# Optimization experiments

Hardware: AMD Instinct MI355X
Metric: run time of the kernel (lower is better)

## Reference

```python
import jax, jax.numpy as jnp
import numpy as np


def setup_inputs() -> dict:
    key = jax.random.key(0)
    k1, k2, k3 = jax.random.split(key, 3)
    N, C, H, W, K = 4, 128, 40, 30, 64
    return {
        "x": jax.random.normal(k1, (N, C, H, W), dtype=jnp.float32),
        "conv_w": jax.random.normal(k2, (K, C), dtype=jnp.float32) * 0.1,  # 1x1 conv weight [K,C,1,1] squeezed
        "centroids": jax.random.uniform(k3, (K, C), dtype=jnp.float32),
        "patch_size": 5,
        "stride": 1,
    }


def reference(x, conv_w, centroids, patch_size, stride):
    N, C, H, W = x.shape
    K = centroids.shape[0]
    # descriptor-wise L2 normalization (torch F.normalize semantics, eps=1e-12)
    norm = jnp.sqrt(jnp.sum(x * x, axis=1, keepdims=True))
    xn = x / jnp.maximum(norm, 1e-12)
    # 1x1 conv (no bias) + softmax over clusters -> soft assignment [N,K,H,W]
    logits = jnp.einsum('nchw,kc->nkhw', xn, conv_w)
    sa = jax.nn.softmax(logits, axis=1)
    # residuals [N,K,C,H,W]: (x - c_k) * a_k, then flatten K,C
    res = (xn[:, None, :, :, :] - centroids[None, :, :, None, None]) * sa[:, :, None, :, :]
    res = res.reshape(N, K * C, H, W)
    # 2D integral image with top-left zero padding -> [N,KC,H+1,W+1]
    I = jnp.cumsum(jnp.cumsum(res, axis=-1), axis=-2)
    I = jnp.pad(I, ((0, 0), (0, 0), (1, 0), (1, 0)))
    # box-filter via integral-image differencing (equivalent to the grouped
    # dilated 2x2 conv with weights [[+1,-1],[-1,+1]], stride=s, dilation=p)
    p, s = int(patch_size), int(stride)
    out = (I[:, :, p::s, p::s] - I[:, :, p::s, :-p:s]
           - I[:, :, :-p:s, p::s] + I[:, :, :-p:s, :-p:s])
    return out / (p * p)
```

## Files before the change

### kernel.cpp

```cpp
#include <hip/hip_runtime.h>

#define C_ 128
#define K_ 64
#define H_ 40
#define W_ 30
#define N_ 4
#define HW_ 1200
#define P_ 5
#define OH_ 36
#define OW_ 26
#define OHW_ 936

template<int CTRL>
__device__ __forceinline__ float dpp0f(float v) {
  return __int_as_float(__builtin_amdgcn_update_dpp(
      0, __float_as_int(v), CTRL, 0xF, 0xF, true));
}
__device__ __forceinline__ float swz_x16(float v) {
  return __int_as_float(__builtin_amdgcn_ds_swizzle(__float_as_int(v), 0x401F));
}

__global__ __launch_bounds__(256) void k1_prep(
    const float* __restrict__ x, const float* __restrict__ cw,
    float* __restrict__ xn, float* __restrict__ sa)
{
  __shared__ float xs[C_][32];
  __shared__ float wt[C_][K_];
  __shared__ float part[8][32];
  __shared__ float ls[K_][32];
  __shared__ float rnorm_s[32];
  __shared__ float rsum_s[32];

  const int tid  = threadIdx.x;
  const int pix0 = blockIdx.x << 5;

  for (int e = tid; e < C_*K_; e += 256) {
    const int c = e >> 6, kk = e & 63;
    wt[c][kk] = cw[kk*C_ + c];
  }
  for (int e = tid; e < C_*32; e += 256) {
    const int c = e >> 5, pl = e & 31;
    const int pix = pix0 + pl;
    const int n = pix / HW_, rem = pix - n*HW_;
    xs[c][pl] = x[(size_t)(n*C_ + c)*HW_ + rem];
  }
  __syncthreads();
  {
    const int pl = tid & 31, cq = tid >> 5;
    float s = 0.f;
    #pragma unroll
    for (int cc = 0; cc < 16; ++cc) {
      const float v = xs[cq*16 + cc][pl];
      s = fmaf(v, v, s);
    }
    part[cq][pl] = s;
  }
  __syncthreads();
  if (tid < 32) {
    float s = 0.f;
    #pragma unroll
    for (int qq = 0; qq < 8; ++qq) s += part[qq][tid];
    rnorm_s[tid] = 1.f / fmaxf(sqrtf(s), 1e-12f);
  }
  __syncthreads();
  {
    const int pl = tid & 31, kq = tid >> 5;
    float acc[8];
    #pragma unroll
    for (int qq = 0; qq < 8; ++qq) acc[qq] = 0.f;
    for (int c = 0; c < C_; ++c) {
      const float xv = xs[c][pl];
      const float4 w0 = *(const float4*)&wt[c][kq*8];
      const float4 w1 = *(const float4*)&wt[c][kq*8 + 4];
      acc[0] = fmaf(xv, w0.x, acc[0]);
      acc[1] = fmaf(xv, w0.y, acc[1]);
      acc[2] = fmaf(xv, w0.z, acc[2]);
      acc[3] = fmaf(xv, w0.w, acc[3]);
      acc[4] = fmaf(xv, w1.x, acc[4]);
      acc[5] = fmaf(xv, w1.y, acc[5]);
      acc[6] = fmaf(xv, w1.z, acc[6]);
      acc[7] = fmaf(xv, w1.w, acc[7]);
    }
    const float rn = rnorm_s[pl];
    #pragma unroll
    for (int qq = 0; qq < 8; ++qq) ls[kq*8 + qq][pl] = acc[qq] * rn;
  }
  __syncthreads();
  if (tid < 32) {
    const int pl = tid;
    float m = -1e30f;
    for (int kk = 0; kk < K_; ++kk) m = fmaxf(m, ls[kk][pl]);
    float s = 0.f;
    for (int kk = 0; kk < K_; ++kk) {
      const float e = expf(ls[kk][pl] - m);
      ls[kk][pl] = e;
      s += e;
    }
    rsum_s[pl] = 1.f / s;
  }
  __syncthreads();
  for (int e = tid; e < K_*32; e += 256) {
    const int kk = e >> 5, pl = e & 31;
    const int pix = pix0 + pl;
    const int n = pix / HW_, rem = pix - n*HW_;
    sa[(size_t)(n*K_ + kk)*HW_ + rem] = ls[kk][pl] * rsum_s[pl];
  }
  for (int e = tid; e < C_*32; e += 256) {
    const int c = e >> 5, pl = e & 31;
    const int pix = pix0 + pl;
    const int n = pix / HW_, rem = pix - n*HW_;
    xn[(size_t)(n*C_ + c)*HW_ + rem] = xs[c][pl] * rnorm_s[pl];
  }
}

__global__ __launch_bounds__(256) void k2_box(
    const float* __restrict__ xn, const float* __restrict__ sa,
    const float* __restrict__ cent, float* __restrict__ out)
{
  const int tid = threadIdx.x;
  const int w   = tid & 31;
  const int wc  = (w < W_) ? w : (W_ - 1);
  const int c   = (blockIdx.x << 3) + (tid >> 5);
  const int k   = blockIdx.y;
  const int n   = blockIdx.z;

  const float cv = cent[k*C_ + c];
  const float* __restrict__ xp = xn + (size_t)(n*C_ + c)*HW_ + wc;
  const float* __restrict__ sp = sa + (size_t)(n*K_ + k)*HW_ + wc;

  float q[H_];
  #pragma unroll
  for (int h = 0; h < H_; ++h) {
    q[h] = (xp[h*W_] - cv) * sp[h*W_];
  }

  float vq = q[0] + q[1] + q[2] + q[3] + q[4];
  float* __restrict__ op = out + (size_t)((n*K_ + k)*C_ + c)*OHW_ + w;

  #pragma unroll
  for (int i = 0; i < OH_; ++i) {
    const float sw = swz_x16(vq);
    float hs = vq;
    hs += dpp0f<0x101>(vq) + dpp0f<0x11F>(sw);
    hs += dpp0f<0x102>(vq) + dpp0f<0x11E>(sw);
    hs += dpp0f<0x103>(vq) + dpp0f<0x11D>(sw);
    hs += dpp0f<0x104>(vq) + dpp0f<0x11C>(sw);
    if (w < OW_) op[i*OW_] = hs * (1.f / (P_*P_));
    if (i < OH_ - 1) vq += q[i + P_] - q[i];
  }
}

extern "C" void kernel_launch(void* const* d_in, const int* in_sizes, int n_in,
                              void* d_out, int out_size, void* d_ws, size_t ws_size,
                              hipStream_t stream) {
  const float* x  = (const float*)d_in[0];
  const float* cw = (const float*)d_in[1];
  const float* ce = (const float*)d_in[2];

  float* xn = (float*)d_ws;
  float* sa = xn + (size_t)N_*C_*HW_;
  float* out = (float*)d_out;

  k1_prep<<<dim3(150), dim3(256), 0, stream>>>(x, cw, xn, sa);
  k2_box<<<dim3(C_/8, K_, N_), dim3(256), 0, stream>>>(xn, sa, ce, out);
}
```

Measured before the change: 46.37 us.

## Restructure prep kernel to 4-pixel blocks with shuffle reductions; fold 1/25 scale

The prep kernel now assigns 4 pixels per block across 1200 blocks instead of 32 pixels across 150. The L2 norm, the logit dot products and the softmax use wave shuffle reductions, and x is read straight from global memory as float4 instead of being staged in LDS. The 1/25 box scale is folded into xn and the centroid, which removes the final multiply in the box kernel. Output stores become nontemporal and the DPP adds are reordered. More blocks improve occupancy on the small prep stage, but x is read from global memory twice and the weights are reloaded by every block.

```diff
diff --git a/kernel.cpp b/kernel.cpp
--- a/kernel.cpp
+++ b/kernel.cpp
@@ -10,6 +10,7 @@
 #define OH_ 36
 #define OW_ 26
 #define OHW_ 936
+#define INV25 (1.0f/25.0f)
 
 template<int CTRL>
 __device__ __forceinline__ float dpp0f(float v) {
@@ -24,92 +25,98 @@
     const float* __restrict__ x, const float* __restrict__ cw,
     float* __restrict__ xn, float* __restrict__ sa)
 {
-  __shared__ float xs[C_][32];
-  __shared__ float wt[C_][K_];
-  __shared__ float part[8][32];
-  __shared__ float ls[K_][32];
-  __shared__ float rnorm_s[32];
-  __shared__ float rsum_s[32];
+  __shared__ float wt[K_][132];
+  __shared__ float ls[K_][5];
 
   const int tid  = threadIdx.x;
-  const int pix0 = blockIdx.x << 5;
+  const int bid  = blockIdx.x;
+  const int n    = bid / 300;
+  const int rem  = (bid - n*300) * 4;
+  const float* __restrict__ xb = x + (size_t)n*C_*HW_ + rem;
 
-  for (int e = tid; e < C_*K_; e += 256) {
-    const int c = e >> 6, kk = e & 63;
-    wt[c][kk] = cw[kk*C_ + c];
+  for (int e = tid; e < K_*C_/4; e += 256) {
+    const int k  = e >> 5;
+    const int c4 = (e & 31) << 2;
+    const float4 v = *(const float4*)(cw + k*C_ + c4);
+    *(float4*)&wt[k][c4] = v;
   }
-  for (int e = tid; e < C_*32; e += 256) {
-    const int c = e >> 5, pl = e & 31;
-    const int pix = pix0 + pl;
-    const int n = pix / HW_, rem = pix - n*HW_;
-    xs[c][pl] = x[(size_t)(n*C_ + c)*HW_ + rem];
+
+  const int lane = tid & 63;
+  const int wv   = tid >> 6;
+  const float4 a0 = *(const float4*)(xb + (size_t)lane*HW_);
+  const float4 a1 = *(const float4*)(xb + (size_t)(lane + 64)*HW_);
+  float sx = a0.x*a0.x + a1.x*a1.x;
+  float sy = a0.y*a0.y + a1.y*a1.y;
+  float sz = a0.z*a0.z + a1.z*a1.z;
+  float sw = a0.w*a0.w + a1.w*a1.w;
+  #pragma unroll
+  for (int m = 1; m < 64; m <<= 1) {
+    sx += __shfl_xor(sx, m, 64);
+    sy += __shfl_xor(sy, m, 64);
+    sz += __shfl_xor(sz, m, 64);
+    sw += __shfl_xor(sw, m, 64);
+  }
+  const float rnx = 1.f / fmaxf(sqrtf(sx), 1e-12f);
+  const float rny = 1.f / fmaxf(sqrtf(sy), 1e-12f);
+  const float rnz = 1.f / fmaxf(sqrtf(sz), 1e-12f);
+  const float rnw = 1.f / fmaxf(sqrtf(sw), 1e-12f);
+
+  if (wv == 0) {
+    float4 o;
+    o.x = a0.x*rnx*INV25; o.y = a0.y*rny*INV25;
+    o.z = a0.z*rnz*INV25; o.w = a0.w*rnw*INV25;
+    *(float4*)(xn + ((size_t)n*C_ + lane)*HW_ + rem) = o;
+  } else if (wv == 1) {
+    float4 o;
+    o.x = a1.x*rnx*INV25; o.y = a1.y*rny*INV25;
+    o.z = a1.z*rnz*INV25; o.w = a1.w*rnw*INV25;
+    *(float4*)(xn + ((size_t)n*C_ + lane + 64)*HW_ + rem) = o;
+  }
+
+  __syncthreads();
+
+  const int k  = tid >> 2;
+  const int cq = tid & 3;
+  const float* __restrict__ xc = xb + (size_t)cq*32*HW_;
+  float ax = 0.f, ay = 0.f, az = 0.f, aw = 0.f;
+  #pragma unroll
+  for (int j = 0; j < 8; ++j) {
+    const float4 w4 = *(const float4*)&wt[k][cq*32 + j*4];
+    const float4 x0 = *(const float4*)(xc + (size_t)(j*4 + 0)*HW_);
+    const float4 x1 = *(const float4*)(xc + (size_t)(j*4 + 1)*HW_);
+    const float4 x2 = *(const float4*)(xc + (size_t)(j*4 + 2)*HW_);
+    const float4 x3 = *(const float4*)(xc + (size_t)(j*4 + 3)*HW_);
+    ax = fmaf(w4.x, x0.x, ax); ay = fmaf(w4.x, x0.y, ay);
+    az = fmaf(w4.x, x0.z, az); aw = fmaf(w4.x, x0.w, aw);
+    ax = fmaf(w4.y, x1.x, ax); ay = fmaf(w4.y, x1.y, ay);
+    az = fmaf(w4.y, x1.z, az); aw = fmaf(w4.y, x1.w, aw);
+    ax = fmaf(w4.z, x2.x, ax); ay = fmaf(w4.z, x2.y, ay);
+    az = fmaf(w4.z, x2.z, az); aw = fmaf(w4.z, x2.w, aw);
+    ax = fmaf(w4.w, x3.x, ax); ay = fmaf(w4.w, x3.y, ay);
+    az = fmaf(w4.w, x3.z, az); aw = fmaf(w4.w, x3.w, aw);
+  }
+  ax += __shfl_xor(ax, 1, 64); ax += __shfl_xor(ax, 2, 64);
+  ay += __shfl_xor(ay, 1, 64); ay += __shfl_xor(ay, 2, 64);
+  az += __shfl_xor(az, 1, 64); az += __shfl_xor(az, 2, 64);
+  aw += __shfl_xor(aw, 1, 64); aw += __shfl_xor(aw, 2, 64);
+  if (cq == 0) {
+    ls[k][0] = ax * rnx;
+    ls[k][1] = ay * rny;
+    ls[k][2] = az * rnz;
+    ls[k][3] = aw * rnw;
   }
   __syncthreads();
+
   {
-    const int pl = tid & 31, cq = tid >> 5;
-    float s = 0.f;
+    const float v = ls[lane][wv];
+    float mx = v;
     #pragma unroll
-    for (int cc = 0; cc < 16; ++cc) {
-      const float v = xs[cq*16 + cc][pl];
-      s = fmaf(v, v, s);
-    }
-    part[cq][pl] = s;
-  }
-  __syncthreads();
-  if (tid < 32) {
-    float s = 0.f;
+    for (int m = 1; m < 64; m <<= 1) mx = fmaxf(mx, __shfl_xor(mx, m, 64));
+    const float e = expf(v - mx);
+    float s = e;
     #pragma unroll
-    for (int qq = 0; qq < 8; ++qq) s += part[qq][tid];
-    rnorm_s[tid] = 1.f / fmaxf(sqrtf(s), 1e-12f);
-  }
-  __syncthreads();
-  {
-    const int pl = tid & 31, kq = tid >> 5;
-    float acc[8];
-    #pragma unroll
-    for (int qq = 0; qq < 8; ++qq) acc[qq] = 0.f;
-    for (int c = 0; c < C_; ++c) {
-      const float xv = xs[c][pl];
-      const float4 w0 = *(const float4*)&wt[c][kq*8];
-      const float4 w1 = *(const float4*)&wt[c][kq*8 + 4];
-      acc[0] = fmaf(xv, w0.x, acc[0]);
-      acc[1] = fmaf(xv, w0.y, acc[1]);
-      acc[2] = fmaf(xv, w0.z, acc[2]);
-      acc[3] = fmaf(xv, w0.w, acc[3]);
-      acc[4] = fmaf(xv, w1.x, acc[4]);
-      acc[5] = fmaf(xv, w1.y, acc[5]);
-      acc[6] = fmaf(xv, w1.z, acc[6]);
-      acc[7] = fmaf(xv, w1.w, acc[7]);
-    }
-    const float rn = rnorm_s[pl];
-    #pragma unroll
-    for (int qq = 0; qq < 8; ++qq) ls[kq*8 + qq][pl] = acc[qq] * rn;
-  }
-  __syncthreads();
-  if (tid < 32) {
-    const int pl = tid;
-    float m = -1e30f;
-    for (int kk = 0; kk < K_; ++kk) m = fmaxf(m, ls[kk][pl]);
-    float s = 0.f;
-    for (int kk = 0; kk < K_; ++kk) {
-      const float e = expf(ls[kk][pl] - m);
-      ls[kk][pl] = e;
-      s += e;
-    }
-    rsum_s[pl] = 1.f / s;
-  }
-  __syncthreads();
-  for (int e = tid; e < K_*32; e += 256) {
-    const int kk = e >> 5, pl = e & 31;
-    const int pix = pix0 + pl;
-    const int n = pix / HW_, rem = pix - n*HW_;
-    sa[(size_t)(n*K_ + kk)*HW_ + rem] = ls[kk][pl] * rsum_s[pl];
-  }
-  for (int e = tid; e < C_*32; e += 256) {
-    const int c = e >> 5, pl = e & 31;
-    const int pix = pix0 + pl;
-    const int n = pix / HW_, rem = pix - n*HW_;
-    xn[(size_t)(n*C_ + c)*HW_ + rem] = xs[c][pl] * rnorm_s[pl];
+    for (int m = 1; m < 64; m <<= 1) s += __shfl_xor(s, m, 64);
+    sa[((size_t)n*K_ + lane)*HW_ + rem + wv] = e / s;
   }
 }
 
@@ -124,14 +131,14 @@
   const int k   = blockIdx.y;
   const int n   = blockIdx.z;
 
-  const float cv = cent[k*C_ + c];
+  const float cv25 = cent[k*C_ + c] * INV25;
   const float* __restrict__ xp = xn + (size_t)(n*C_ + c)*HW_ + wc;
   const float* __restrict__ sp = sa + (size_t)(n*K_ + k)*HW_ + wc;
 
   float q[H_];
   #pragma unroll
   for (int h = 0; h < H_; ++h) {
-    q[h] = (xp[h*W_] - cv) * sp[h*W_];
+    q[h] = (xp[h*W_] - cv25) * sp[h*W_];
   }
 
   float vq = q[0] + q[1] + q[2] + q[3] + q[4];
@@ -141,11 +148,15 @@
   for (int i = 0; i < OH_; ++i) {
     const float sw = swz_x16(vq);
     float hs = vq;
-    hs += dpp0f<0x101>(vq) + dpp0f<0x11F>(sw);
-    hs += dpp0f<0x102>(vq) + dpp0f<0x11E>(sw);
-    hs += dpp0f<0x103>(vq) + dpp0f<0x11D>(sw);
-    hs += dpp0f<0x104>(vq) + dpp0f<0x11C>(sw);
-    if (w < OW_) op[i*OW_] = hs * (1.f / (P_*P_));
+    hs += dpp0f<0x101>(vq);
+    hs += dpp0f<0x102>(vq);
+    hs += dpp0f<0x103>(vq);
+    hs += dpp0f<0x104>(vq);
+    hs += dpp0f<0x11F>(sw);
+    hs += dpp0f<0x11E>(sw);
+    hs += dpp0f<0x11D>(sw);
+    hs += dpp0f<0x11C>(sw);
+    if (w < OW_) __builtin_nontemporal_store(hs, &op[i*OW_]);
     if (i < OH_ - 1) vq += q[i + P_] - q[i];
   }
 }
@@ -161,6 +172,6 @@
   float* sa = xn + (size_t)N_*C_*HW_;
   float* out = (float*)d_out;
 
-  k1_prep<<<dim3(150), dim3(256), 0, stream>>>(x, cw, xn, sa);
+  k1_prep<<<dim3(1200), dim3(256), 0, stream>>>(x, cw, xn, sa);
   k2_box<<<dim3(C_/8, K_, N_), dim3(256), 0, stream>>>(xn, sa, ce, out);
 }
```

New measurement: 91.98 us. 98.4% more time.

## Shrink prep tile to 8 pixels, use wave-shuffle softmax, 600 blocks

Applied to the files above, without the earlier changes.

The prep kernel now processes 8 pixels per block instead of 32, launching 600 blocks instead of 150 so more CUs are occupied. The logits matmul is split so each thread computes 2 clusters. The serial single-warp softmax is replaced by a per-wave shuffle reduction over the 64 clusters. Shared-memory weight rows are padded to reduce bank conflicts. In exchange, each block reloads the full weight matrix, giving 4x more redundant weight traffic, and the second kernel, which likely dominates runtime, is unchanged.

```diff
diff --git a/kernel.cpp b/kernel.cpp
--- a/kernel.cpp
+++ b/kernel.cpp
@@ -24,92 +24,80 @@
     const float* __restrict__ x, const float* __restrict__ cw,
     float* __restrict__ xn, float* __restrict__ sa)
 {
-  __shared__ float xs[C_][32];
-  __shared__ float wt[C_][K_];
-  __shared__ float part[8][32];
-  __shared__ float ls[K_][32];
-  __shared__ float rnorm_s[32];
-  __shared__ float rsum_s[32];
+  __shared__ float xs[C_][8];
+  __shared__ float wt[C_][66];
+  __shared__ float part[32][8];
+  __shared__ float ls[K_][9];
+  __shared__ float rnorm_s[8];
 
-  const int tid  = threadIdx.x;
-  const int pix0 = blockIdx.x << 5;
+  const int tid = threadIdx.x;
+  const int bid = blockIdx.x;
+  const int n   = bid / 150;
+  const int rem = (bid - n*150) * 8;
 
   for (int e = tid; e < C_*K_; e += 256) {
     const int c = e >> 6, kk = e & 63;
     wt[c][kk] = cw[kk*C_ + c];
   }
-  for (int e = tid; e < C_*32; e += 256) {
-    const int c = e >> 5, pl = e & 31;
-    const int pix = pix0 + pl;
-    const int n = pix / HW_, rem = pix - n*HW_;
-    xs[c][pl] = x[(size_t)(n*C_ + c)*HW_ + rem];
+  for (int e = tid; e < C_*8; e += 256) {
+    const int c = e >> 3, p2 = e & 7;
+    xs[c][p2] = x[((size_t)n*C_ + c)*HW_ + rem + p2];
   }
   __syncthreads();
+
+  const int pl = tid & 7;
+  const int kq = tid >> 3;
   {
-    const int pl = tid & 31, cq = tid >> 5;
     float s = 0.f;
     #pragma unroll
-    for (int cc = 0; cc < 16; ++cc) {
-      const float v = xs[cq*16 + cc][pl];
+    for (int cc = 0; cc < 4; ++cc) {
+      const float v = xs[kq*4 + cc][pl];
       s = fmaf(v, v, s);
     }
-    part[cq][pl] = s;
+    part[kq][pl] = s;
   }
   __syncthreads();
-  if (tid < 32) {
+  if (tid < 8) {
     float s = 0.f;
     #pragma unroll
-    for (int qq = 0; qq < 8; ++qq) s += part[qq][tid];
+    for (int q = 0; q < 32; ++q) s += part[q][tid];
     rnorm_s[tid] = 1.f / fmaxf(sqrtf(s), 1e-12f);
   }
   __syncthreads();
+
   {
-    const int pl = tid & 31, kq = tid >> 5;
-    float acc[8];
-    #pragma unroll
-    for (int qq = 0; qq < 8; ++qq) acc[qq] = 0.f;
+    float a0 = 0.f, a1 = 0.f;
+    #pragma unroll 8
     for (int c = 0; c < C_; ++c) {
       const float xv = xs[c][pl];
-      const float4 w0 = *(const float4*)&wt[c][kq*8];
-      const float4 w1 = *(const float4*)&wt[c][kq*8 + 4];
-      acc[0] = fmaf(xv, w0.x, acc[0]);
-      acc[1] = fmaf(xv, w0.y, acc[1]);
-      acc[2] = fmaf(xv, w0.z, acc[2]);
-      acc[3] = fmaf(xv, w0.w, acc[3]);
-      acc[4] = fmaf(xv, w1.x, acc[4]);
-      acc[5] = fmaf(xv, w1.y, acc[5]);
-      acc[6] = fmaf(xv, w1.z, acc[6]);
-      acc[7] = fmaf(xv, w1.w, acc[7]);
+      const float2 w2 = *(const float2*)&wt[c][kq*2];
+      a0 = fmaf(xv, w2.x, a0);
+      a1 = fmaf(xv, w2.y, a1);
     }
     const float rn = rnorm_s[pl];
-    #pragma unroll
-    for (int qq = 0; qq < 8; ++qq) ls[kq*8 + qq][pl] = acc[qq] * rn;
+    ls[kq*2 + 0][pl] = a0 * rn;
+    ls[kq*2 + 1][pl] = a1 * rn;
+  }
+  for (int e = tid; e < C_*8; e += 256) {
+    const int c = e >> 3, p2 = e & 7;
+    xn[((size_t)n*C_ + c)*HW_ + rem + p2] = xs[c][p2] * rnorm_s[p2];
   }
   __syncthreads();
-  if (tid < 32) {
-    const int pl = tid;
-    float m = -1e30f;
-    for (int kk = 0; kk < K_; ++kk) m = fmaxf(m, ls[kk][pl]);
-    float s = 0.f;
-    for (int kk = 0; kk < K_; ++kk) {
-      const float e = expf(ls[kk][pl] - m);
-      ls[kk][pl] = e;
-      s += e;
-    }
-    rsum_s[pl] = 1.f / s;
-  }
-  __syncthreads();
-  for (int e = tid; e < K_*32; e += 256) {
-    const int kk = e >> 5, pl = e & 31;
-    const int pix = pix0 + pl;
-    const int n = pix / HW_, rem = pix - n*HW_;
-    sa[(size_t)(n*K_ + kk)*HW_ + rem] = ls[kk][pl] * rsum_s[pl];
-  }
-  for (int e = tid; e < C_*32; e += 256) {
-    const int c = e >> 5, pl = e & 31;
-    const int pix = pix0 + pl;
-    const int n = pix / HW_, rem = pix - n*HW_;
-    xn[(size_t)(n*C_ + c)*HW_ + rem] = xs[c][pl] * rnorm_s[pl];
+
+  const int lane = tid & 63;
+  const int wv   = tid >> 6;
+  #pragma unroll
+  for (int r = 0; r < 2; ++r) {
+    const int p = wv + (r << 2);
+    const float v = ls[lane][p];
+    float mx = v;
+    #pragma unroll
+    for (int m = 1; m < 64; m <<= 1) mx = fmaxf(mx, __shfl_xor(mx, m, 64));
+    const float e = expf(v - mx);
+    float s = e;
+    #pragma unroll
+    for (int m = 1; m < 64; m <<= 1) s += __shfl_xor(s, m, 64);
+    sa[((size_t)n*K_ + lane)*HW_ + rem + p] = e / s;
   }
 }
 
@@ -161,6 +149,6 @@
   float* sa = xn + (size_t)N_*C_*HW_;
   float* out = (float*)d_out;
 
-  k1_prep<<<dim3(150), dim3(256), 0, stream>>>(x, cw, xn, sa);
+  k1_prep<<<dim3(600), dim3(256), 0, stream>>>(x, cw, xn, sa);
   k2_box<<<dim3(C_/8, K_, N_), dim3(256), 0, stream>>>(xn, sa, ce, out);
 }
```

New measurement: 51.21 us. 1.1x slower.
